# Kernel optimization log

Hardware: AMD Instinct MI355X
Metric: run time of the kernel (lower is better)

## Reference

```python
import jax, jax.numpy as jnp
import numpy as np

N = 100000      # nodes
E = 1600000     # edges (before self-loops)
F_IN = 128      # num_features
H = 4           # heads
C = 32          # out_channels per head (num_hidden)
SLOPE = 0.2     # leaky relu negative slope (alpha)


def setup_inputs() -> dict:
    key = jax.random.key(0)
    k = jax.random.split(key, 6)
    x = jax.random.normal(k[0], (N, F_IN), jnp.float32)
    edge_index = jax.random.randint(k[1], (2, E), 0, N, dtype=jnp.int64)
    W = jax.random.normal(k[2], (F_IN, H * C), jnp.float32) * (1.0 / np.sqrt(F_IN))
    att_src = jax.random.normal(k[3], (H, C), jnp.float32) * 0.1
    att_dst = jax.random.normal(k[4], (H, C), jnp.float32) * 0.1
    bias = jnp.zeros((H * C,), jnp.float32)
    return dict(x=x, W=W, att_src=att_src, att_dst=att_dst, bias=bias,
                edge_index=edge_index)


def reference(x, W, att_src, att_dst, bias, edge_index):
    # PyG GATConv (concat=True, add_self_loops=True), eval mode (dropout off).
    loops = jnp.arange(N, dtype=edge_index.dtype)
    ei = jnp.concatenate([edge_index, jnp.stack([loops, loops])], axis=1)
    src, dst = ei[0], ei[1]                     # [E+N]

    h = (x @ W).reshape(N, H, C)                # projected node features
    a_src = jnp.einsum('nhc,hc->nh', h, att_src)   # [N, H]
    a_dst = jnp.einsum('nhc,hc->nh', h, att_dst)   # [N, H]

    e = a_src[src] + a_dst[dst]                 # [E+N, H]
    e = jnp.where(e > 0, e, SLOPE * e)          # leaky relu

    # segment softmax over incoming edges of each dst node (per head)
    m = jax.lax.stop_gradient(jax.ops.segment_max(e, dst, num_segments=N))
    p = jnp.exp(e - m[dst])
    denom = jax.ops.segment_sum(p, dst, num_segments=N)
    alpha = p / (denom[dst] + 1e-16)            # [E+N, H]

    # weighted scatter-aggregate of source features
    out = jax.ops.segment_sum(alpha[:, :, None] * h[src], dst, num_segments=N)
    return out.reshape(N, H * C) + bias
```

## Files before the change

### kernel.cpp

```cpp
#include <hip/hip_runtime.h>
#include <hip/hip_bf16.h>
#include <math.h>

#define N_NODES 100000
#define F_IN    128
#define HC      128
#define NH      4
#define SLOPE   0.2f

#define NB      196
#define BSH     9
#define CAP     10240
#define CHUNK   8192
#define PADK    136

typedef __attribute__((ext_vector_type(8))) short short8;
typedef __attribute__((ext_vector_type(4))) float f32x4;
typedef __attribute__((ext_vector_type(2))) float fx2;

static __device__ __forceinline__ float leaky(float x) { return x > 0.f ? x : SLOPE * x; }

static __device__ __forceinline__ short f2bs(float f) {
    __hip_bfloat16 b = __float2bfloat16(f);
    return *reinterpret_cast<short*>(&b);
}

__global__ __launch_bounds__(256) void k_gemm(const float* __restrict__ x,
                                              const float* __restrict__ W,
                                              const float* __restrict__ att_src,
                                              const float* __restrict__ att_dst,
                                              unsigned short* __restrict__ hb,
                                              float* __restrict__ a_src,
                                              float* __restrict__ a_dst)
{
    __shared__ short xs[64 * PADK];
    __shared__ short ws[128 * PADK];
    const int t  = threadIdx.x;
    const int r0 = blockIdx.x * 64;

    for (int i = t; i < 2048; i += 256) {
        int row = i >> 5, kq = (i & 31) * 4;
        int gr = r0 + row;
        float4 v = make_float4(0.f, 0.f, 0.f, 0.f);
        if (gr < N_NODES) v = ((const float4*)(x + (size_t)gr * F_IN))[i & 31];
        short* p = &xs[row * PADK + kq];
        p[0] = f2bs(v.x); p[1] = f2bs(v.y); p[2] = f2bs(v.z); p[3] = f2bs(v.w);
    }
    for (int i = t; i < 4096; i += 256) {
        int k = i >> 5, nq = (i & 31) * 4;
        float4 v = *(const float4*)&W[k * HC + nq];
        ws[(nq + 0) * PADK + k] = f2bs(v.x);
        ws[(nq + 1) * PADK + k] = f2bs(v.y);
        ws[(nq + 2) * PADK + k] = f2bs(v.z);
        ws[(nq + 3) * PADK + k] = f2bs(v.w);
    }
    __syncthreads();

    const int wave = t >> 6, lane = t & 63;
    const int quad = lane >> 4, l16 = lane & 15;
    const int wrow = wave * 16;

    f32x4 acc[8];
    #pragma unroll
    for (int nt = 0; nt < 8; ++nt) acc[nt] = (f32x4){0.f, 0.f, 0.f, 0.f};

    const short* ap = &xs[(wrow + l16) * PADK + quad * 8];
    #pragma unroll
    for (int kb = 0; kb < 4; ++kb) {
        short8 a = *(const short8*)(ap + kb * 32);
        #pragma unroll
        for (int nt = 0; nt < 8; ++nt) {
            short8 b = *(const short8*)&ws[(nt * 16 + l16) * PADK + kb * 32 + quad * 8];
            acc[nt] = __builtin_amdgcn_mfma_f32_16x16x32_bf16(a, b, acc[nt], 0, 0, 0);
        }
    }

    float att_s[8], att_d[8];
    #pragma unroll
    for (int nt = 0; nt < 8; ++nt) {
        att_s[nt] = att_src[nt * 16 + l16];
        att_d[nt] = att_dst[nt * 16 + l16];
    }

    #pragma unroll
    for (int g = 0; g < 4; ++g) {
        int r = r0 + wrow + quad * 4 + g;
        if (r < N_NODES) {
            #pragma unroll
            for (int nt = 0; nt < 8; ++nt)
                hb[(size_t)r * HC + nt * 16 + l16] = (unsigned short)f2bs(acc[nt][g]);
        }
        float s0 = acc[0][g] * att_s[0] + acc[1][g] * att_s[1];
        float s1 = acc[2][g] * att_s[2] + acc[3][g] * att_s[3];
        float s2 = acc[4][g] * att_s[4] + acc[5][g] * att_s[5];
        float s3 = acc[6][g] * att_s[6] + acc[7][g] * att_s[7];
        float d0 = acc[0][g] * att_d[0] + acc[1][g] * att_d[1];
        float d1 = acc[2][g] * att_d[2] + acc[3][g] * att_d[3];
        float d2 = acc[4][g] * att_d[4] + acc[5][g] * att_d[5];
        float d3 = acc[6][g] * att_d[6] + acc[7][g] * att_d[7];
        #pragma unroll
        for (int o = 1; o < 16; o <<= 1) {
            s0 += __shfl_xor(s0, o); s1 += __shfl_xor(s1, o);
            s2 += __shfl_xor(s2, o); s3 += __shfl_xor(s3, o);
            d0 += __shfl_xor(d0, o); d1 += __shfl_xor(d1, o);
            d2 += __shfl_xor(d2, o); d3 += __shfl_xor(d3, o);
        }
        if (l16 == 0 && r < N_NODES) {
            *(float4*)&a_src[r * NH] = make_float4(s0, s1, s2, s3);
            *(float4*)&a_dst[r * NH] = make_float4(d0, d1, d2, d3);
        }
    }
}

__global__ __launch_bounds__(256) void k_bucket(const int* __restrict__ srcp,
                                                const int* __restrict__ dstp,
                                                int* __restrict__ bucket_cursor,
                                                int* __restrict__ eb, int E)
{
    __shared__ int ebuf[CHUNK];
    __shared__ unsigned char bkt[CHUNK];
    __shared__ int hist[256];
    __shared__ int lexcl[257];
    __shared__ int gbase[256];
    __shared__ int sdata[256];

    const int t = threadIdx.x;
    const int base = blockIdx.x * CHUNK;

    hist[t] = 0;
    __syncthreads();

    #pragma unroll
    for (int j = 0; j < CHUNK / 256; ++j) {
        int i = base + t + j * 256;
        if (i < E) atomicAdd(&hist[dstp[i] >> BSH], 1);
    }
    __syncthreads();

    int cnt = hist[t];
    sdata[t] = cnt;
    __syncthreads();
    for (int o = 1; o < 256; o <<= 1) {
        int add = (t >= o) ? sdata[t - o] : 0;
        __syncthreads();
        sdata[t] += add;
        __syncthreads();
    }
    int excl = sdata[t] - cnt;
    lexcl[t] = excl;
    if (t == 255) lexcl[256] = sdata[255];
    hist[t] = excl;
    int gb = 0;
    if (t < NB && cnt > 0) gb = atomicAdd(&bucket_cursor[t], cnt);
    gbase[t] = t * CAP + gb;
    __syncthreads();

    #pragma unroll
    for (int j = 0; j < CHUNK / 256; ++j) {
        int i = base + t + j * 256;
        if (i < E) {
            int s = srcp[i], d = dstp[i];
            int b = d >> BSH;
            int r = atomicAdd(&hist[b], 1);
            ebuf[r] = (s << BSH) | (d & 511);
            bkt[r] = (unsigned char)b;
        }
    }
    __syncthreads();

    const int blockTotal = lexcl[256];
    for (int i = t; i < blockTotal; i += 256) {
        int b = bkt[i];
        eb[gbase[b] + (i - lexcl[b])] = ebuf[i];
    }
}

__global__ void k_bscan(const int* __restrict__ bucket_cursor,
                        int* __restrict__ bexcl)
{
    __shared__ int sdata[256];
    const int t = threadIdx.x;
    int nvalid = 0;
    if (t < NB) {
        int n0 = t * 512;
        nvalid = min(512, N_NODES - n0);
        if (nvalid < 0) nvalid = 0;
    }
    int v = (t < NB) ? bucket_cursor[t] + nvalid : 0;
    sdata[t] = v;
    __syncthreads();
    for (int o = 1; o < 256; o <<= 1) {
        int add = (t >= o) ? sdata[t - o] : 0;
        __syncthreads();
        sdata[t] += add;
        __syncthreads();
    }
    if (t < NB) bexcl[t] = sdata[t] - v;
}

__global__ __launch_bounds__(256) void k_csr(const int* __restrict__ eb,
                                             const int* __restrict__ bucket_cursor,
                                             const int* __restrict__ bexcl,
                                             int* __restrict__ col,
                                             int2* __restrict__ rowse)
{
    __shared__ int deg[512];
    __shared__ int sdata[256];

    const int t  = threadIdx.x;
    const int b  = blockIdx.x;
    const int n0 = b * 512;
    const int cnt   = bucket_cursor[b];
    const int ebase = b * CAP;
    const int gofs  = bexcl[b];

    deg[t]       = (n0 + t       < N_NODES) ? 1 : 0;
    deg[t + 256] = (n0 + t + 256 < N_NODES) ? 1 : 0;
    __syncthreads();

    for (int i = t; i < cnt; i += 256)
        atomicAdd(&deg[eb[ebase + i] & 511], 1);
    __syncthreads();

    int d0 = deg[2 * t], d1 = deg[2 * t + 1];
    int ps = d0 + d1;
    sdata[t] = ps;
    __syncthreads();
    for (int o = 1; o < 256; o <<= 1) {
        int add = (t >= o) ? sdata[t - o] : 0;
        __syncthreads();
        sdata[t] += add;
        __syncthreads();
    }
    int e0 = sdata[t] - ps;
    int e1 = e0 + d0;
    __syncthreads();

    int na = n0 + 2 * t, nb2 = n0 + 2 * t + 1;
    if (na < N_NODES) {
        rowse[na] = make_int2(gofs + e0, gofs + e0 + d0);
        col[gofs + e0] = na;
    }
    if (nb2 < N_NODES) {
        rowse[nb2] = make_int2(gofs + e1, gofs + e1 + d1);
        col[gofs + e1] = nb2;
    }
    deg[2 * t]     = e0 + 1;
    deg[2 * t + 1] = e1 + 1;
    __syncthreads();

    for (int i = t; i < cnt; i += 256) {
        int v = eb[ebase + i];
        int r = atomicAdd(&deg[v & 511], 1);
        col[gofs + r] = v >> BSH;
    }
}

__global__ __launch_bounds__(256) void k_node(const unsigned short* __restrict__ hb,
                                              const float* __restrict__ a_src,
                                              const float* __restrict__ a_dst,
                                              const int2* __restrict__ rowse,
                                              const int* __restrict__ col,
                                              const float* __restrict__ bias,
                                              float* __restrict__ out)
{
    const int lane = threadIdx.x & 63;
    const int node = blockIdx.x * 4 + (threadIdx.x >> 6);
    if (node >= N_NODES) return;

    const int2 se = rowse[node];
    const int r0 = se.x, r1 = se.y;
    const int myh = lane >> 4;
    const float adm = a_dst[node * NH + myh];

    float denom = 0.f, acc0 = 0.f, acc1 = 0.f;
    int i = r0;
    for (; i + 8 <= r1; i += 8) {
        int s[8];
        #pragma unroll
        for (int j = 0; j < 8; ++j) s[j] = col[i + j];
        float as[8];
        #pragma unroll
        for (int j = 0; j < 8; ++j) as[j] = a_src[s[j] * NH + myh];
        unsigned int hv[8];
        #pragma unroll
        for (int j = 0; j < 8; ++j)
            hv[j] = *(const unsigned int*)&hb[(size_t)s[j] * HC + 2 * lane];
        #pragma unroll
        for (int j = 0; j < 8; ++j) {
            float p = __expf(leaky(as[j] + adm));
            denom += p;
            acc0 += p * __uint_as_float(hv[j] << 16);
            acc1 += p * __uint_as_float(hv[j] & 0xffff0000u);
        }
    }
    for (; i < r1; ++i) {
        int s = col[i];
        float p = __expf(leaky(a_src[s * NH + myh] + adm));
        unsigned int v = *(const unsigned int*)&hb[(size_t)s * HC + 2 * lane];
        denom += p;
        acc0 += p * __uint_as_float(v << 16);
        acc1 += p * __uint_as_float(v & 0xffff0000u);
    }

    float inv = 1.f / (denom + 1e-16f);
    fx2 o2;
    o2.x = acc0 * inv + bias[2 * lane];
    o2.y = acc1 * inv + bias[2 * lane + 1];
    __builtin_nontemporal_store(o2, (fx2*)&out[(size_t)node * HC + 2 * lane]);
}

extern "C" void kernel_launch(void* const* d_in, const int* in_sizes, int n_in,
                              void* d_out, int out_size, void* d_ws, size_t ws_size,
                              hipStream_t stream)
{
    const float* x       = (const float*)d_in[0];
    const float* W       = (const float*)d_in[1];
    const float* att_src = (const float*)d_in[2];
    const float* att_dst = (const float*)d_in[3];
    const float* bias    = (const float*)d_in[4];
    const int*   ei      = (const int*)d_in[5];
    const int E = in_sizes[5] / 2;
    const int* srcp = ei;
    const int* dstp = ei + E;
    float* out = (float*)d_out;

    char* wsb = (char*)d_ws;
    size_t off = 0;
    auto alloc = [&](size_t bytes) -> char* {
        char* p = wsb + off;
        off += (bytes + 255) & ~(size_t)255;
        return p;
    };
    unsigned short* hb = (unsigned short*)alloc((size_t)N_NODES * HC * sizeof(unsigned short));
    float* a_src   = (float*)alloc((size_t)N_NODES * NH * sizeof(float));
    float* a_dst   = (float*)alloc((size_t)N_NODES * NH * sizeof(float));
    int*   eb      = (int*)alloc((size_t)NB * CAP * sizeof(int));
    int*   col     = (int*)alloc((size_t)(E + N_NODES) * sizeof(int));
    int2*  rowse   = (int2*)alloc((size_t)N_NODES * sizeof(int2));
    int*   bcursor = (int*)alloc(256 * sizeof(int));
    int*   bexcl   = (int*)alloc(256 * sizeof(int));

    (void)hipMemsetAsync(bcursor, 0, 256 * sizeof(int), stream);

    k_gemm<<<(N_NODES + 63) / 64, 256, 0, stream>>>(x, W, att_src, att_dst,
                                                    hb, a_src, a_dst);
    k_bucket<<<(E + CHUNK - 1) / CHUNK, 256, 0, stream>>>(srcp, dstp, bcursor, eb, E);
    k_bscan<<<1, 256, 0, stream>>>(bcursor, bexcl);
    k_csr<<<NB, 256, 0, stream>>>(eb, bcursor, bexcl, col, rowse);
    k_node<<<(N_NODES + 3) / 4, 256, 0, stream>>>(hb, a_src, a_dst, rowse, col, bias, out);
}
```

Measured before the change: 291.6 us.

## Build CSR with global atomic degree count and scan; pretranspose W once

Replaces the two-pass bucketed CSR construction, which staged edges through shared-memory buckets and did per-bucket counting, with a direct approach. A global atomic degree histogram feeds a three-kernel prefix scan, and a scatter pass then places each source index using a global atomic cursor per destination. It also adds a small kernel that converts and transposes W to bf16 once, so each GEMM block copies it with vector loads instead of redoing the transposed scalar writes. The trade is many contended or random global atomics and uncoalesced col writes, plus more kernel launches, in place of shared-memory-local work.

```diff
diff --git a/kernel.cpp b/kernel.cpp
--- a/kernel.cpp
+++ b/kernel.cpp
@@ -8,11 +8,8 @@
 #define NH      4
 #define SLOPE   0.2f
 
-#define NB      196
-#define BSH     9
-#define CAP     10240
-#define CHUNK   8192
 #define PADK    136
+#define NSB     98
 
 typedef __attribute__((ext_vector_type(8))) short short8;
 typedef __attribute__((ext_vector_type(4))) float f32x4;
@@ -25,8 +22,18 @@
     return *reinterpret_cast<short*>(&b);
 }
 
+__global__ __launch_bounds__(256) void k_prep(const float* __restrict__ W,
+                                              unsigned short* __restrict__ wt)
+{
+    int t = blockIdx.x * 256 + threadIdx.x;
+    if (t < 128 * 128) {
+        int k = t >> 7, n = t & 127;
+        wt[n * 128 + k] = (unsigned short)f2bs(W[k * HC + n]);
+    }
+}
+
 __global__ __launch_bounds__(256) void k_gemm(const float* __restrict__ x,
-                                              const float* __restrict__ W,
+                                              const unsigned short* __restrict__ wt,
                                               const float* __restrict__ att_src,
                                               const float* __restrict__ att_dst,
                                               unsigned short* __restrict__ hb,
@@ -46,13 +53,9 @@
         short* p = &xs[row * PADK + kq];
         p[0] = f2bs(v.x); p[1] = f2bs(v.y); p[2] = f2bs(v.z); p[3] = f2bs(v.w);
     }
-    for (int i = t; i < 4096; i += 256) {
-        int k = i >> 5, nq = (i & 31) * 4;
-        float4 v = *(const float4*)&W[k * HC + nq];
-        ws[(nq + 0) * PADK + k] = f2bs(v.x);
-        ws[(nq + 1) * PADK + k] = f2bs(v.y);
-        ws[(nq + 2) * PADK + k] = f2bs(v.z);
-        ws[(nq + 3) * PADK + k] = f2bs(v.w);
+    for (int i = t; i < 2048; i += 256) {
+        int n = i >> 4, k0 = (i & 15) * 8;
+        *(float4*)&ws[n * PADK + k0] = *(const float4*)&wt[n * 128 + k0];
     }
     __syncthreads();
 
@@ -112,147 +115,82 @@
     }
 }
 
-__global__ __launch_bounds__(256) void k_bucket(const int* __restrict__ srcp,
-                                                const int* __restrict__ dstp,
-                                                int* __restrict__ bucket_cursor,
-                                                int* __restrict__ eb, int E)
-{
-    __shared__ int ebuf[CHUNK];
-    __shared__ unsigned char bkt[CHUNK];
-    __shared__ int hist[256];
-    __shared__ int lexcl[257];
-    __shared__ int gbase[256];
-    __shared__ int sdata[256];
-
+__global__ __launch_bounds__(256) void k_deg(const int* __restrict__ dstp,
+                                             int* __restrict__ deg, int E)
+{
+    int i = blockIdx.x * 2048 + threadIdx.x;
+    #pragma unroll
+    for (int j = 0; j < 8; ++j, i += 256)
+        if (i < E) atomicAdd(&deg[dstp[i]], 1);
+}
+
+__global__ __launch_bounds__(1024) void k_scanA(const int* __restrict__ deg,
+                                                int* __restrict__ dx,
+                                                int* __restrict__ btot)
+{
+    __shared__ int sdata[1024];
+    const int t = threadIdx.x, b = blockIdx.x;
+    const int n = b * 1024 + t;
+    int v = (n < N_NODES) ? (deg[n] + 1) : 0;
+    sdata[t] = v;
+    __syncthreads();
+    for (int o = 1; o < 1024; o <<= 1) {
+        int add = (t >= o) ? sdata[t - o] : 0;
+        __syncthreads();
+        sdata[t] += add;
+        __syncthreads();
+    }
+    if (n < N_NODES) dx[n] = sdata[t] - v;
+    if (t == 1023) btot[b] = sdata[1023];
+}
+
+__global__ void k_scanB(const int* __restrict__ btot, int* __restrict__ bofs)
+{
+    __shared__ int sdata[128];
     const int t = threadIdx.x;
-    const int base = blockIdx.x * CHUNK;
-
-    hist[t] = 0;
+    int v = (t < NSB) ? btot[t] : 0;
+    sdata[t] = v;
     __syncthreads();
-
-    #pragma unroll
-    for (int j = 0; j < CHUNK / 256; ++j) {
-        int i = base + t + j * 256;
-        if (i < E) atomicAdd(&hist[dstp[i] >> BSH], 1);
-    }
-    __syncthreads();
-
-    int cnt = hist[t];
-    sdata[t] = cnt;
-    __syncthreads();
-    for (int o = 1; o < 256; o <<= 1) {
+    for (int o = 1; o < 128; o <<= 1) {
         int add = (t >= o) ? sdata[t - o] : 0;
         __syncthreads();
         sdata[t] += add;
         __syncthreads();
     }
-    int excl = sdata[t] - cnt;
-    lexcl[t] = excl;
-    if (t == 255) lexcl[256] = sdata[255];
-    hist[t] = excl;
-    int gb = 0;
-    if (t < NB && cnt > 0) gb = atomicAdd(&bucket_cursor[t], cnt);
-    gbase[t] = t * CAP + gb;
-    __syncthreads();
-
-    #pragma unroll
-    for (int j = 0; j < CHUNK / 256; ++j) {
-        int i = base + t + j * 256;
+    if (t < NSB) bofs[t] = sdata[t] - v;
+}
+
+__global__ __launch_bounds__(1024) void k_scanC(const int* __restrict__ deg,
+                                                const int* __restrict__ dx,
+                                                const int* __restrict__ bofs,
+                                                int2* __restrict__ rowse,
+                                                int* __restrict__ col,
+                                                int* __restrict__ cursor)
+{
+    const int t = threadIdx.x, b = blockIdx.x;
+    const int n = b * 1024 + t;
+    if (n < N_NODES) {
+        int start = bofs[b] + dx[n];
+        int d = deg[n];
+        rowse[n] = make_int2(start, start + d + 1);
+        col[start] = n;
+        cursor[n] = start + 1;
+    }
+}
+
+__global__ __launch_bounds__(256) void k_scatter(const int* __restrict__ srcp,
+                                                 const int* __restrict__ dstp,
+                                                 int* __restrict__ cursor,
+                                                 int* __restrict__ col, int E)
+{
+    int i = blockIdx.x * 2048 + threadIdx.x;
+    #pragma unroll
+    for (int j = 0; j < 8; ++j, i += 256) {
         if (i < E) {
             int s = srcp[i], d = dstp[i];
-            int b = d >> BSH;
-            int r = atomicAdd(&hist[b], 1);
-            ebuf[r] = (s << BSH) | (d & 511);
-            bkt[r] = (unsigned char)b;
-        }
-    }
-    __syncthreads();
-
-    const int blockTotal = lexcl[256];
-    for (int i = t; i < blockTotal; i += 256) {
-        int b = bkt[i];
-        eb[gbase[b] + (i - lexcl[b])] = ebuf[i];
-    }
-}
-
-__global__ void k_bscan(const int* __restrict__ bucket_cursor,
-                        int* __restrict__ bexcl)
-{
-    __shared__ int sdata[256];
-    const int t = threadIdx.x;
-    int nvalid = 0;
-    if (t < NB) {
-        int n0 = t * 512;
-        nvalid = min(512, N_NODES - n0);
-        if (nvalid < 0) nvalid = 0;
-    }
-    int v = (t < NB) ? bucket_cursor[t] + nvalid : 0;
-    sdata[t] = v;
-    __syncthreads();
-    for (int o = 1; o < 256; o <<= 1) {
-        int add = (t >= o) ? sdata[t - o] : 0;
-        __syncthreads();
-        sdata[t] += add;
-        __syncthreads();
-    }
-    if (t < NB) bexcl[t] = sdata[t] - v;
-}
-
-__global__ __launch_bounds__(256) void k_csr(const int* __restrict__ eb,
-                                             const int* __restrict__ bucket_cursor,
-                                             const int* __restrict__ bexcl,
-                                             int* __restrict__ col,
-                                             int2* __restrict__ rowse)
-{
-    __shared__ int deg[512];
-    __shared__ int sdata[256];
-
-    const int t  = threadIdx.x;
-    const int b  = blockIdx.x;
-    const int n0 = b * 512;
-    const int cnt   = bucket_cursor[b];
-    const int ebase = b * CAP;
-    const int gofs  = bexcl[b];
-
-    deg[t]       = (n0 + t       < N_NODES) ? 1 : 0;
-    deg[t + 256] = (n0 + t + 256 < N_NODES) ? 1 : 0;
-    __syncthreads();
-
-    for (int i = t; i < cnt; i += 256)
-        atomicAdd(&deg[eb[ebase + i] & 511], 1);
-    __syncthreads();
-
-    int d0 = deg[2 * t], d1 = deg[2 * t + 1];
-    int ps = d0 + d1;
-    sdata[t] = ps;
-    __syncthreads();
-    for (int o = 1; o < 256; o <<= 1) {
-        int add = (t >= o) ? sdata[t - o] : 0;
-        __syncthreads();
-        sdata[t] += add;
-        __syncthreads();
-    }
-    int e0 = sdata[t] - ps;
-    int e1 = e0 + d0;
-    __syncthreads();
-
-    int na = n0 + 2 * t, nb2 = n0 + 2 * t + 1;
-    if (na < N_NODES) {
-        rowse[na] = make_int2(gofs + e0, gofs + e0 + d0);
-        col[gofs + e0] = na;
-    }
-    if (nb2 < N_NODES) {
-        rowse[nb2] = make_int2(gofs + e1, gofs + e1 + d1);
-        col[gofs + e1] = nb2;
-    }
-    deg[2 * t]     = e0 + 1;
-    deg[2 * t + 1] = e1 + 1;
-    __syncthreads();
-
-    for (int i = t; i < cnt; i += 256) {
-        int v = eb[ebase + i];
-        int r = atomicAdd(&deg[v & 511], 1);
-        col[gofs + r] = v >> BSH;
+            int r = atomicAdd(&cursor[d], 1);
+            col[r] = s;
+        }
     }
 }
 
@@ -335,18 +273,26 @@
     unsigned short* hb = (unsigned short*)alloc((size_t)N_NODES * HC * sizeof(unsigned short));
     float* a_src   = (float*)alloc((size_t)N_NODES * NH * sizeof(float));
     float* a_dst   = (float*)alloc((size_t)N_NODES * NH * sizeof(float));
-    int*   eb      = (int*)alloc((size_t)NB * CAP * sizeof(int));
     int*   col     = (int*)alloc((size_t)(E + N_NODES) * sizeof(int));
     int2*  rowse   = (int2*)alloc((size_t)N_NODES * sizeof(int2));
-    int*   bcursor = (int*)alloc(256 * sizeof(int));
-    int*   bexcl   = (int*)alloc(256 * sizeof(int));
-
-    (void)hipMemsetAsync(bcursor, 0, 256 * sizeof(int), stream);
-
-    k_gemm<<<(N_NODES + 63) / 64, 256, 0, stream>>>(x, W, att_src, att_dst,
+    int*   deg     = (int*)alloc((size_t)N_NODES * sizeof(int));
+    int*   dx      = (int*)alloc((size_t)N_NODES * sizeof(int));
+    int*   cursor  = (int*)alloc((size_t)N_NODES * sizeof(int));
+    int*   btot    = (int*)alloc(128 * sizeof(int));
+    int*   bofs    = (int*)alloc(128 * sizeof(int));
+    unsigned short* wt = (unsigned short*)alloc(128 * 128 * sizeof(unsigned short));
+
+    (void)hipMemsetAsync(deg, 0, (size_t)N_NODES * sizeof(int), stream);
+
+    const int egrid = (E + 2047) / 2048;
+
+    k_prep<<<64, 256, 0, stream>>>(W, wt);
+    k_gemm<<<(N_NODES + 63) / 64, 256, 0, stream>>>(x, wt, att_src, att_dst,
                                                     hb, a_src, a_dst);
-    k_bucket<<<(E + CHUNK - 1) / CHUNK, 256, 0, stream>>>(srcp, dstp, bcursor, eb, E);
-    k_bscan<<<1, 256, 0, stream>>>(bcursor, bexcl);
-    k_csr<<<NB, 256, 0, stream>>>(eb, bcursor, bexcl, col, rowse);
+    k_deg<<<egrid, 256, 0, stream>>>(dstp, deg, E);
+    k_scanA<<<NSB, 1024, 0, stream>>>(deg, dx, btot);
+    k_scanB<<<1, 128, 0, stream>>>(btot, bofs);
+    k_scanC<<<NSB, 1024, 0, stream>>>(deg, dx, bofs, rowse, col, cursor);
+    k_scatter<<<egrid, 256, 0, stream>>>(srcp, dstp, cursor, col, E);
     k_node<<<(N_NODES + 3) / 4, 256, 0, stream>>>(hb, a_src, a_dst, rowse, col, bias, out);
 }
```

Measured after the change: 381.2 us. 1.31x slower.
